# Kernel optimization log

Measured on AMD Instinct MI355X. Metric: run time of the kernel, lower is better.

The kernel has to match this reference:

```python
import jax, jax.numpy as jnp
import numpy as np

C_EXP = 8.0  # fixed gate sharpness from the module (self.c = 8.0)

def setup_inputs() -> dict:
    key = jax.random.key(0)
    k1, k2, k3, k4 = jax.random.split(key, 4)
    B, T, D = 8, 4096, 1024
    x = jax.random.normal(k1, (B, T, D), dtype=jnp.float32)
    W_r = jax.random.normal(k2, (D, D), dtype=jnp.float32) * (1.0 / np.sqrt(D))
    W_i = jax.random.normal(k3, (D, D), dtype=jnp.float32) * (1.0 / np.sqrt(D))
    lambd = jax.random.normal(k4, (D,), dtype=jnp.float32)
    return {"x": x, "W_r": W_r, "W_i": W_i, "lambd": lambd}

def reference(x, W_r, W_i, lambd):
    # Gates (nn.Linear with bias=False: y = x @ W.T)
    r = jax.nn.sigmoid(jnp.einsum('btd,ed->bte', x, W_r))
    i = jax.nn.sigmoid(jnp.einsum('btd,ed->bte', x, W_i))
    # a = sigmoid(lambd) ** (c * r), computed stably in log space
    log_a = C_EXP * r * jax.nn.log_sigmoid(lambd)  # [B,T,D], log_a <= 0
    a = jnp.exp(log_a)
    # input-normalized injection: sqrt(1 - a^2) * (i * x)
    b = jnp.sqrt(jnp.maximum(1.0 - jnp.exp(2.0 * log_a), 0.0)) * (i * x)
    # linear recurrence h_t = a_t * h_{t-1} + b_t via associative scan over T
    def combine(c1, c2):
        a1, b1 = c1
        a2, b2 = c2
        return (a1 * a2, a2 * b1 + b2)
    _, h = jax.lax.associative_scan(combine, (a, b), axis=1)
    return h
```

## Files before the change

kernel.cpp:

```cpp
#include <hip/hip_runtime.h>
#include <hip/hip_bf16.h>
#include <cstdint>

#define B_   8
#define T_   4096
#define D_   1024
#define M_   (B_*T_)
#define K_   D_
#define N_   D_

#define TC   128
#define NC   (T_/TC)

#define BM   128
#define BN   128
#define BK   64

typedef __attribute__((ext_vector_type(8))) short  short8;
typedef __attribute__((ext_vector_type(4))) float  floatx4;

#define XB_OFF    0ull
#define WR_OFF    (XB_OFF + (size_t)M_*K_*2)
#define WI_OFF    (WR_OFF + (size_t)N_*K_*2)
#define LS_OFF    (WI_OFF + (size_t)N_*K_*2)
#define ASUM_OFF  (LS_OFF + (size_t)D_*4)
#define ESUM_OFF  (ASUM_OFF + (size_t)B_*NC*D_*4)
#define WS_NEED   (ESUM_OFF + (size_t)B_*NC*D_*4)

__device__ __forceinline__ uint32_t f2bf(float f) {
  uint32_t u = __float_as_uint(f);
  return (u + 0x7fffu + ((u >> 16) & 1u)) >> 16;
}

__device__ __forceinline__ void gload_lds16(const void* g, void* l) {
  __builtin_amdgcn_global_load_lds(
      (const __attribute__((address_space(1))) void*)g,
      (__attribute__((address_space(3))) void*)l, 16, 0, 0);
}

__global__ __launch_bounds__(256) void convert_kernel(
    const float* __restrict__ x, const float* __restrict__ wr,
    const float* __restrict__ wi, const float* __restrict__ lambd,
    uint2* __restrict__ xb, uint2* __restrict__ wrb, uint2* __restrict__ wib,
    float* __restrict__ ls) {
  int gid = blockIdx.x * 256 + threadIdx.x;
  if (gid < D_) {
    float l = lambd[gid];
    ls[gid] = fminf(l, 0.f) - log1pf(__expf(-fabsf(l)));
  }
  const int XQ = M_*K_/4;
  const int WQ = N_*K_/4;
  int stride = gridDim.x * 256;
  for (int q = gid; q < XQ + 2*WQ; q += stride) {
    const float4* src; uint2* dst; int i;
    if (q < XQ)           { src = (const float4*)x;  dst = xb;  i = q; }
    else if (q < XQ + WQ) { src = (const float4*)wr; dst = wrb; i = q - XQ; }
    else                  { src = (const float4*)wi; dst = wib; i = q - XQ - WQ; }
    float4 v = src[i];
    uint2 o;
    o.x = (f2bf(v.y) << 16) | f2bf(v.x);
    o.y = (f2bf(v.w) << 16) | f2bf(v.z);
    dst[i] = o;
  }
}

__global__ __launch_bounds__(256, 2) void dual_gemm_kernel(
    const short* __restrict__ xb, const short* __restrict__ wrb,
    const short* __restrict__ wib, const float* __restrict__ ls,
    uint32_t* __restrict__ ab) {
  __shared__ short lds[(BM + 2*BN) * BK];
  short* As  = lds;
  short* Brs = lds + BM*BK;
  short* Bis = lds + 2*BM*BK;

  const int tid  = threadIdx.x;
  const int lane = tid & 63;
  const int wv   = tid >> 6;
  const int wm   = wv >> 1;
  const int wn   = wv & 1;
  const int c16  = lane & 15;
  const int q    = lane >> 4;

  const int bm = blockIdx.x * BM;
  const int bn = blockIdx.y * BN;

  floatx4 accR[4][4], accI[4][4];
  #pragma unroll
  for (int i = 0; i < 4; ++i)
    #pragma unroll
    for (int j = 0; j < 4; ++j) {
      accR[i][j] = (floatx4){0.f,0.f,0.f,0.f};
      accI[i][j] = (floatx4){0.f,0.f,0.f,0.f};
    }

  const int srow0  = wv*32 + (lane >> 3);
  const int schunk = lane & 7;

  for (int k0 = 0; k0 < K_; k0 += BK) {
    #pragma unroll
    for (int l = 0; l < 4; ++l) {
      int r  = srow0 + l*8;
      int cc = schunk ^ (r & 7);
      size_t goff = (size_t)k0 + cc*8;
      gload_lds16(xb  + (size_t)(bm + r)*K_ + goff, As  + wv*2048 + l*512);
      gload_lds16(wrb + (size_t)(bn + r)*K_ + goff, Brs + wv*2048 + l*512);
      gload_lds16(wib + (size_t)(bn + r)*K_ + goff, Bis + wv*2048 + l*512);
    }
    __syncthreads();

    #pragma unroll
    for (int kk = 0; kk < BK/32; ++kk) {
      short8 af[4], brf[4], bif[4];
      #pragma unroll
      for (int f = 0; f < 4; ++f) {
        int m_loc = wm*64 + f*16 + c16;
        int cph   = (kk*4 + q) ^ (m_loc & 7);
        af[f]  = *(const short8*)(As  + m_loc*64 + cph*8);
        int n_loc = wn*64 + f*16 + c16;
        int cphn  = (kk*4 + q) ^ (n_loc & 7);
        brf[f] = *(const short8*)(Brs + n_loc*64 + cphn*8);
        bif[f] = *(const short8*)(Bis + n_loc*64 + cphn*8);
      }
      #pragma unroll
      for (int fm = 0; fm < 4; ++fm)
        #pragma unroll
        for (int fn = 0; fn < 4; ++fn) {
          accR[fm][fn] = __builtin_amdgcn_mfma_f32_16x16x32_bf16(
              af[fm], brf[fn], accR[fm][fn], 0, 0, 0);
          accI[fm][fn] = __builtin_amdgcn_mfma_f32_16x16x32_bf16(
              af[fm], bif[fn], accI[fm][fn], 0, 0, 0);
        }
    }
    __syncthreads();
  }

  #pragma unroll
  for (int fn = 0; fn < 4; ++fn) {
    int col = bn + wn*64 + fn*16 + c16;
    float lsv = ls[col];
    #pragma unroll
    for (int fm = 0; fm < 4; ++fm) {
      #pragma unroll
      for (int j = 0; j < 4; ++j) {
        int row = bm + wm*64 + fm*16 + q*4 + j;
        float pr = accR[fm][fn][j];
        float pi = accI[fm][fn][j];
        float rg = 1.f / (1.f + __expf(-pr));
        float ig = 1.f / (1.f + __expf(-pi));
        float la = 8.f * rg * lsv;
        uint32_t xu = (uint32_t)(uint16_t)xb[(size_t)row*K_ + col];
        float xv = __uint_as_float(xu << 16);
        float a2 = __expf(2.f * la);
        float bb = sqrtf(fmaxf(1.f - a2, 0.f)) * ig * xv;
        ab[(size_t)row*N_ + col] = (f2bf(bb) << 16) | f2bf(la);
      }
    }
  }
}

__global__ __launch_bounds__(256) void scan_summary(
    const uint32_t* __restrict__ ab, float* __restrict__ Asum,
    float* __restrict__ Esum) {
  int blk = blockIdx.x;
  int dg = blk & 3;
  int c  = (blk >> 2) & (NC - 1);
  int b  = blk >> 7;
  int d  = (dg << 8) + threadIdx.x;
  const uint32_t* p = ab + ((size_t)(b*T_ + c*TC))*D_ + d;
  float A = 1.f, h = 0.f;
  #pragma unroll 4
  for (int t = 0; t < TC; ++t) {
    uint32_t v = p[(size_t)t * D_];
    float a  = __expf(__uint_as_float(v << 16));
    float bb = __uint_as_float(v & 0xffff0000u);
    A *= a;
    h = fmaf(a, h, bb);
  }
  int o = (b*NC + c)*D_ + d;
  Asum[o] = A;
  Esum[o] = h;
}

__global__ __launch_bounds__(256) void scan_carry(
    float* __restrict__ Asum, const float* __restrict__ Esum) {
  int b = blockIdx.x >> 2;
  int d = ((blockIdx.x & 3) << 8) + threadIdx.x;
  float carry = 0.f;
  for (int c = 0; c < NC; ++c) {
    int o = (b*NC + c)*D_ + d;
    float A = Asum[o], E = Esum[o];
    Asum[o] = carry;
    carry = fmaf(A, carry, E);
  }
}

__global__ __launch_bounds__(256) void scan_final(
    uint32_t* __restrict__ out, const float* __restrict__ carry_buf) {
  int blk = blockIdx.x;
  int dg = blk & 3;
  int c  = (blk >> 2) & (NC - 1);
  int b  = blk >> 7;
  int d  = (dg << 8) + threadIdx.x;

  float h = carry_buf[(b*NC + c)*D_ + d];

  uint32_t* p = out + ((size_t)(b*T_ + c*TC))*D_ + d;
  #pragma unroll 4
  for (int t = 0; t < TC; ++t) {
    size_t o = (size_t)t * D_;
    uint32_t v = p[o];
    float a = __expf(__uint_as_float(v << 16));
    h = fmaf(a, h, __uint_as_float(v & 0xffff0000u));
    p[o] = __float_as_uint(h);
  }
}

extern "C" void kernel_launch(void* const* d_in, const int* in_sizes, int n_in,
                              void* d_out, int out_size, void* d_ws, size_t ws_size,
                              hipStream_t stream) {
  (void)in_sizes; (void)n_in; (void)out_size;
  if (ws_size < WS_NEED) return;

  const float* x     = (const float*)d_in[0];
  const float* Wr    = (const float*)d_in[1];
  const float* Wi    = (const float*)d_in[2];
  const float* lambd = (const float*)d_in[3];

  char* ws = (char*)d_ws;
  short* xb   = (short*)(ws + XB_OFF);
  short* wrb  = (short*)(ws + WR_OFF);
  short* wib  = (short*)(ws + WI_OFF);
  float* ls   = (float*)(ws + LS_OFF);
  float* Asum = (float*)(ws + ASUM_OFF);
  float* Esum = (float*)(ws + ESUM_OFF);

  uint32_t* ab = (uint32_t*)d_out;

  convert_kernel<<<4096, 256, 0, stream>>>(x, Wr, Wi, lambd,
                                           (uint2*)xb, (uint2*)wrb, (uint2*)wib, ls);
  dual_gemm_kernel<<<dim3(M_/BM, N_/BN), 256, 0, stream>>>(xb, wrb, wib, ls, ab);
  scan_summary<<<B_ * NC * (D_/256), 256, 0, stream>>>(ab, Asum, Esum);
  scan_carry<<<B_ * 4, 256, 0, stream>>>(Asum, Esum);
  scan_final<<<B_ * NC * (D_/256), 256, 0, stream>>>(ab, Asum);
}
```

Baseline: 453.3 us.

## Fuse chunk scan summaries into GEMM epilogue and vectorize final scan

Computes per-64-row chunk (A,E) summaries directly in the dual GEMM epilogue using per-thread serial combines and cross-lane shuffles, removing the separate scan_summary kernel and its full re-read of the packed a/b buffer. The chunk size is halved to match each wave's 64-row tile, which doubles the length of the sequential carry pass. The final scan kernel now processes two columns per thread with 8-byte vector loads and stores. The epilogue gains extra exp and shuffle work, which may add register pressure.

```diff
diff --git a/kernel.cpp b/kernel.cpp
--- a/kernel.cpp
+++ b/kernel.cpp
@@ -9,8 +9,8 @@
 #define K_   D_
 #define N_   D_
 
-#define TC   128
-#define NC   (T_/TC)
+#define TC2  64
+#define NC2  (T_/TC2)
 
 #define BM   128
 #define BN   128
@@ -24,8 +24,8 @@
 #define WI_OFF    (WR_OFF + (size_t)N_*K_*2)
 #define LS_OFF    (WI_OFF + (size_t)N_*K_*2)
 #define ASUM_OFF  (LS_OFF + (size_t)D_*4)
-#define ESUM_OFF  (ASUM_OFF + (size_t)B_*NC*D_*4)
-#define WS_NEED   (ESUM_OFF + (size_t)B_*NC*D_*4)
+#define ESUM_OFF  (ASUM_OFF + (size_t)B_*NC2*D_*4)
+#define WS_NEED   (ESUM_OFF + (size_t)B_*NC2*D_*4)
 
 __device__ __forceinline__ uint32_t f2bf(float f) {
   uint32_t u = __float_as_uint(f);
@@ -67,7 +67,8 @@
 __global__ __launch_bounds__(256, 2) void dual_gemm_kernel(
     const short* __restrict__ xb, const short* __restrict__ wrb,
     const short* __restrict__ wib, const float* __restrict__ ls,
-    uint32_t* __restrict__ ab) {
+    uint32_t* __restrict__ ab, float* __restrict__ Asum,
+    float* __restrict__ Esum) {
   __shared__ short lds[(BM + 2*BN) * BK];
   short* As  = lds;
   short* Brs = lds + BM*BK;
@@ -134,12 +135,16 @@
     __syncthreads();
   }
 
+  const int b_idx = bm >> 12;
+  const int c2    = ((bm & (T_-1)) >> 6) + wm;
   #pragma unroll
   for (int fn = 0; fn < 4; ++fn) {
     int col = bn + wn*64 + fn*16 + c16;
     float lsv = ls[col];
+    float WA = 1.f, WE = 0.f;
     #pragma unroll
     for (int fm = 0; fm < 4; ++fm) {
+      float SA = 1.f, SE = 0.f;
       #pragma unroll
       for (int j = 0; j < 4; ++j) {
         int row = bm + wm*64 + fm*16 + q*4 + j;
@@ -152,33 +157,30 @@
         float xv = __uint_as_float(xu << 16);
         float a2 = __expf(2.f * la);
         float bb = sqrtf(fmaxf(1.f - a2, 0.f)) * ig * xv;
-        ab[(size_t)row*N_ + col] = (f2bf(bb) << 16) | f2bf(la);
+        uint32_t pk = (f2bf(bb) << 16) | f2bf(la);
+        ab[(size_t)row*N_ + col] = pk;
+        float av  = __expf(__uint_as_float(pk << 16));
+        float bbr = __uint_as_float(pk & 0xffff0000u);
+        SA *= av;
+        SE = fmaf(av, SE, bbr);
       }
-    }
-  }
-}
-
-__global__ __launch_bounds__(256) void scan_summary(
-    const uint32_t* __restrict__ ab, float* __restrict__ Asum,
-    float* __restrict__ Esum) {
-  int blk = blockIdx.x;
-  int dg = blk & 3;
-  int c  = (blk >> 2) & (NC - 1);
-  int b  = blk >> 7;
-  int d  = (dg << 8) + threadIdx.x;
-  const uint32_t* p = ab + ((size_t)(b*T_ + c*TC))*D_ + d;
-  float A = 1.f, h = 0.f;
-  #pragma unroll 4
-  for (int t = 0; t < TC; ++t) {
-    uint32_t v = p[(size_t)t * D_];
-    float a  = __expf(__uint_as_float(v << 16));
-    float bb = __uint_as_float(v & 0xffff0000u);
-    A *= a;
-    h = fmaf(a, h, bb);
-  }
-  int o = (b*NC + c)*D_ + d;
-  Asum[o] = A;
-  Esum[o] = h;
+      #pragma unroll
+      for (int s = 16; s <= 32; s <<= 1) {
+        float OA = __shfl_xor(SA, s);
+        float OE = __shfl_xor(SE, s);
+        SE = (lane & s) ? fmaf(SA, OE, SE)
+                        : fmaf(OA, SE, OE);
+        SA *= OA;
+      }
+      WE = fmaf(SA, WE, SE);
+      WA *= SA;
+    }
+    if (q == 0) {
+      int o = (b_idx * NC2 + c2) * D_ + col;
+      Asum[o] = WA;
+      Esum[o] = WE;
+    }
+  }
 }
 
 __global__ __launch_bounds__(256) void scan_carry(
@@ -186,8 +188,9 @@
   int b = blockIdx.x >> 2;
   int d = ((blockIdx.x & 3) << 8) + threadIdx.x;
   float carry = 0.f;
-  for (int c = 0; c < NC; ++c) {
-    int o = (b*NC + c)*D_ + d;
+  #pragma unroll 8
+  for (int c = 0; c < NC2; ++c) {
+    int o = (b*NC2 + c)*D_ + d;
     float A = Asum[o], E = Esum[o];
     Asum[o] = carry;
     carry = fmaf(A, carry, E);
@@ -197,21 +200,26 @@
 __global__ __launch_bounds__(256) void scan_final(
     uint32_t* __restrict__ out, const float* __restrict__ carry_buf) {
   int blk = blockIdx.x;
-  int dg = blk & 3;
-  int c  = (blk >> 2) & (NC - 1);
+  int dg = blk & 1;
+  int c  = (blk >> 1) & (NC2 - 1);
   int b  = blk >> 7;
-  int d  = (dg << 8) + threadIdx.x;
-
-  float h = carry_buf[(b*NC + c)*D_ + d];
-
-  uint32_t* p = out + ((size_t)(b*T_ + c*TC))*D_ + d;
+  int d2 = (dg << 8) + threadIdx.x;
+
+  const float2* cb = (const float2*)(carry_buf + (size_t)(b*NC2 + c)*D_);
+  float2 hc = cb[d2];
+  float h0 = hc.x, h1 = hc.y;
+
+  uint2* p = (uint2*)(out + ((size_t)(b*T_ + c*TC2))*D_) + d2;
   #pragma unroll 4
-  for (int t = 0; t < TC; ++t) {
-    size_t o = (size_t)t * D_;
-    uint32_t v = p[o];
-    float a = __expf(__uint_as_float(v << 16));
-    h = fmaf(a, h, __uint_as_float(v & 0xffff0000u));
-    p[o] = __float_as_uint(h);
+  for (int t = 0; t < TC2; ++t) {
+    size_t o = (size_t)t * (D_/2);
+    uint2 v = p[o];
+    float a0 = __expf(__uint_as_float(v.x << 16));
+    h0 = fmaf(a0, h0, __uint_as_float(v.x & 0xffff0000u));
+    float a1 = __expf(__uint_as_float(v.y << 16));
+    h1 = fmaf(a1, h1, __uint_as_float(v.y & 0xffff0000u));
+    uint2 ov; ov.x = __float_as_uint(h0); ov.y = __float_as_uint(h1);
+    p[o] = ov;
   }
 }
 
@@ -238,8 +246,8 @@
 
   convert_kernel<<<4096, 256, 0, stream>>>(x, Wr, Wi, lambd,
                                            (uint2*)xb, (uint2*)wrb, (uint2*)wib, ls);
-  dual_gemm_kernel<<<dim3(M_/BM, N_/BN), 256, 0, stream>>>(xb, wrb, wib, ls, ab);
-  scan_summary<<<B_ * NC * (D_/256), 256, 0, stream>>>(ab, Asum, Esum);
+  dual_gemm_kernel<<<dim3(M_/BM, N_/BN), 256, 0, stream>>>(xb, wrb, wib, ls, ab,
+                                                           Asum, Esum);
   scan_carry<<<B_ * 4, 256, 0, stream>>>(Asum, Esum);
-  scan_final<<<B_ * NC * (D_/256), 256, 0, stream>>>(ab, Asum);
-}
+  scan_final<<<B_ * NC2 * 2, 256, 0, stream>>>(ab, Asum);
+}
```

New measurement: 445.6 us. About the same (-1.7%).
